# Optimization experiments

Measured on AMD Instinct MI355X. Metric: run time of the kernel, lower is better.

The kernel has to match this reference:

```python
import jax, jax.numpy as jnp
import numpy as np

NUM_USERS = 50000
NUM_ITEMS = 50000
EMBED_DIM = 128
NUM_LAYERS = 3
NUM_EDGES = 600000
N_NODES = NUM_USERS + NUM_ITEMS


def setup_inputs() -> dict:
    key = jax.random.key(0)
    k1, k2, k3, k4, k5 = jax.random.split(key, 5)
    edge_index = jax.random.randint(k1, (2, NUM_EDGES), 0, N_NODES, dtype=jnp.int64 if jax.config.x64_enabled else jnp.int32)
    user_emb = jax.random.normal(k2, (NUM_USERS, EMBED_DIM), jnp.float32) * 0.1
    item_emb = jax.random.normal(k3, (NUM_ITEMS, EMBED_DIM), jnp.float32) * 0.1
    Wa = jax.random.normal(k4, (NUM_LAYERS, 2 * EMBED_DIM, 1), jnp.float32) * 0.05
    ba = jnp.zeros((NUM_LAYERS, 1), jnp.float32)
    Wg = jax.random.normal(k5, (NUM_LAYERS, 2 * EMBED_DIM, EMBED_DIM), jnp.float32) * 0.05
    bg = jnp.zeros((NUM_LAYERS, EMBED_DIM), jnp.float32)
    return {"edge_index": edge_index, "user_emb": user_emb, "item_emb": item_emb,
            "Wa": Wa, "ba": ba, "Wg": Wg, "bg": bg}


def reference(edge_index, user_emb, item_emb, Wa, ba, Wg, bg):
    U = user_emb.shape[0]
    N = U + item_emb.shape[0]
    src, dst = edge_index[0], edge_index[1]
    x = jnp.concatenate([user_emb, item_emb], axis=0)  # [N, d]
    for l in range(Wa.shape[0]):
        src_emb = x[src]                                # [E, d] gather
        dst_emb = x[dst]                                # [E, d] gather
        cat = jnp.concatenate([src_emb, dst_emb], 1)    # [E, 2d]
        att = jax.nn.sigmoid(cat @ Wa[l] + ba[l])       # [E, 1]
        # attention-weighted scatter-sum over destination node (zeros for isolated nodes)
        agg = jax.ops.segment_sum(src_emb * att, dst, num_segments=N)  # [N, d]
        x = jax.nn.relu(jnp.concatenate([x, agg], 1) @ Wg[l] + bg[l])  # [N, d]
    return x[:U], x[U:]
```

## Files before the change

kernel.cpp:

```cpp
#include <hip/hip_runtime.h>
#include <cstddef>
#include <cstdint>

#define NUSERS 50000
#define NITEMS 50000
#define NNODES 100000
#define DIM    128
#define NLAYERS 3
#define NEDGES 600000
#define NPAD 100096

#define EBLK  8192
#define NBLK  74
#define NBUCK 782

#define PRO_CONCAT 6250
#define PRO_WG     48
#define PRO_TOTAL  (PRO_CONCAT + PRO_WG + NBLK)

typedef __attribute__((ext_vector_type(8))) short short8;
typedef __attribute__((ext_vector_type(4))) float f32x4;

__device__ __forceinline__ float bf_lo(unsigned u) { return __uint_as_float(u << 16); }
__device__ __forceinline__ float bf_hi(unsigned u) { return __uint_as_float(u & 0xffff0000u); }
__device__ __forceinline__ unsigned short f2bf(float f) {
    unsigned b = __float_as_uint(f);
    return (unsigned short)((b + 0x7fffu + ((b >> 16) & 1u)) >> 16);
}
__device__ __forceinline__ unsigned pack2(float lo, float hi) {
    return ((unsigned)f2bf(hi) << 16) | (unsigned)f2bf(lo);
}

__device__ __forceinline__ void async16(const void* g, void* l) {
    __builtin_amdgcn_global_load_lds(
        (const __attribute__((address_space(1))) unsigned int*)(uintptr_t)g,
        (__attribute__((address_space(3))) unsigned int*)(unsigned int)(uintptr_t)l,
        16, 0, 0);
}

__global__ __launch_bounds__(256) void prologue_kernel(
        const float* __restrict__ ue, const float* __restrict__ ie,
        const float* __restrict__ Wa, const float* __restrict__ ba,
        const float* __restrict__ Wg, const int* __restrict__ dst,
        unsigned short* __restrict__ xb,
        float* __restrict__ a_src, float* __restrict__ a_dst,
        unsigned short* __restrict__ Bf, unsigned* __restrict__ counts) {
    __shared__ unsigned hist[NBUCK];
    const int blk = blockIdx.x;

    if (blk < PRO_CONCAT) {
        const int n = blk * 16 + (threadIdx.x >> 4);
        if (n >= NNODES) return;
        const int sub = threadIdx.x & 15;
        const float* r = (n < NUSERS) ? (ue + (size_t)n * DIM)
                                      : (ie + (size_t)(n - NUSERS) * DIM);
        const float4 v0 = *(const float4*)(r + sub * 8);
        const float4 v1 = *(const float4*)(r + sub * 8 + 4);
        const float4 wl0 = *(const float4*)(Wa + sub * 8);
        const float4 wl1 = *(const float4*)(Wa + sub * 8 + 4);
        const float4 wh0 = *(const float4*)(Wa + DIM + sub * 8);
        const float4 wh1 = *(const float4*)(Wa + DIM + sub * 8 + 4);

        uint4 o;
        o.x = pack2(v0.x, v0.y);
        o.y = pack2(v0.z, v0.w);
        o.z = pack2(v1.x, v1.y);
        o.w = pack2(v1.z, v1.w);
        *(uint4*)(xb + (size_t)n * DIM + sub * 8) = o;

        float ps = v0.x * wl0.x + v0.y * wl0.y + v0.z * wl0.z + v0.w * wl0.w
                 + v1.x * wl1.x + v1.y * wl1.y + v1.z * wl1.z + v1.w * wl1.w;
        float pd = v0.x * wh0.x + v0.y * wh0.y + v0.z * wh0.z + v0.w * wh0.w
                 + v1.x * wh1.x + v1.y * wh1.y + v1.z * wh1.z + v1.w * wh1.w;
        #pragma unroll
        for (int off = 1; off < 16; off <<= 1) {
            ps += __shfl_xor(ps, off);
            pd += __shfl_xor(pd, off);
        }
        if (sub == 0) { a_src[n] = ps; a_dst[n] = pd + ba[0]; }
    } else if (blk < PRO_CONCAT + PRO_WG) {
        const int tid = (blk - PRO_CONCAT) * 256 + threadIdx.x;
        if (tid >= NLAYERS * 4096) return;
        const int l    = tid >> 12;
        const int slot = tid & 4095;
        const int lane = slot & 63;
        const int t2   = slot >> 6;
        const int nf   = t2 & 3;
        const int t3   = t2 >> 2;
        const int ks   = t3 & 7;
        const int nb   = t3 >> 3;
        const int col  = nb * 64 + nf * 16 + (lane & 15);
        const int k0   = ks * 32 + (lane >> 4) * 8;
        const float* wsrc = Wg + (size_t)l * 256 * DIM;
        unsigned short o[8];
        #pragma unroll
        for (int j = 0; j < 8; ++j) o[j] = f2bf(wsrc[(size_t)(k0 + j) * DIM + col]);
        *(short8*)(Bf + (size_t)tid * 8) = *(short8*)o;
    } else {
        const int bblk = blk - PRO_CONCAT - PRO_WG;
        for (int i = threadIdx.x; i < NBUCK; i += 256) hist[i] = 0;
        __syncthreads();
        const int base = bblk * EBLK;
        const int end  = (base + EBLK < NEDGES) ? base + EBLK : NEDGES;
        for (int e = base + threadIdx.x; e < end; e += 256)
            atomicAdd(&hist[dst[e] >> 7], 1u);
        __syncthreads();
        for (int i = threadIdx.x; i < NBUCK; i += 256)
            counts[(size_t)bblk * NBUCK + i] = hist[i];
    }
}

__global__ __launch_bounds__(256) void scan_blocks_kernel(
        unsigned* __restrict__ counts, unsigned* __restrict__ totals) {
    const int b = blockIdx.x * 4 + (threadIdx.x >> 6);
    if (b >= NBUCK) return;
    const int l = threadIdx.x & 63;

    const unsigned c0 = counts[(size_t)l * NBUCK + b];
    const unsigned c1 = (64 + l < NBLK)
                        ? counts[(size_t)(64 + l) * NBUCK + b] : 0;

    unsigned s0 = c0, s1 = c1;
    #pragma unroll
    for (int o = 1; o < 64; o <<= 1) {
        const unsigned t0 = (unsigned)__shfl_up((int)s0, o);
        const unsigned t1 = (unsigned)__shfl_up((int)s1, o);
        if (l >= o) { s0 += t0; s1 += t1; }
    }
    const unsigned tot0 = (unsigned)__shfl((int)s0, 63);
    const unsigned tot1 = (unsigned)__shfl((int)s1, NBLK - 65);

    counts[(size_t)l * NBUCK + b] = s0 - c0;
    if (64 + l < NBLK)
        counts[(size_t)(64 + l) * NBUCK + b] = tot0 + s1 - c1;
    if (l == 0) totals[b] = tot0 + tot1;
}

__global__ __launch_bounds__(1024) void bucketbase_kernel(
        const unsigned* __restrict__ totals, unsigned* __restrict__ bucketbase) {
    const int b = threadIdx.x;
    const unsigned v = (b < NBUCK) ? totals[b] : 0u;
    const int lane = b & 63, w = b >> 6;
    unsigned s = v;
    #pragma unroll
    for (int o = 1; o < 64; o <<= 1) {
        const unsigned t = (unsigned)__shfl_up((int)s, o);
        if (lane >= o) s += t;
    }
    __shared__ unsigned wsum[16];
    if (lane == 63) wsum[w] = s;
    __syncthreads();
    unsigned add = 0;
    #pragma unroll
    for (int j = 0; j < 15; ++j) if (w > j) add += wsum[j];
    if (b < NBUCK) bucketbase[b] = s + add - v;
    if (b == NBUCK - 1) bucketbase[NBUCK] = s + add;
}

__global__ __launch_bounds__(256) void bin_scatter_kernel(
        const int* __restrict__ src, const int* __restrict__ dst,
        const unsigned* __restrict__ counts, const unsigned* __restrict__ bucketbase,
        unsigned* __restrict__ pairs) {
    __shared__ unsigned off[NBUCK];
    for (int i = threadIdx.x; i < NBUCK; i += 256)
        off[i] = bucketbase[i] + counts[(size_t)blockIdx.x * NBUCK + i];
    __syncthreads();
    const int base = blockIdx.x * EBLK;
    const int end  = (base + EBLK < NEDGES) ? base + EBLK : NEDGES;
    for (int e = base + threadIdx.x; e < end; e += 256) {
        const int d = dst[e];
        const unsigned pos = atomicAdd(&off[d >> 7], 1u);
        pairs[pos] = ((unsigned)(d & 127) << 17) | (unsigned)src[e];
    }
}

__global__ __launch_bounds__(256) void bucket_csr_kernel(
        const unsigned* __restrict__ pairs, const unsigned* __restrict__ bucketbase,
        int* __restrict__ row_start, int* __restrict__ csr_src) {
    __shared__ unsigned deg[128], fill[128], wtot[2];
    const int b = blockIdx.x;
    const unsigned seg0 = bucketbase[b], seg1 = bucketbase[b + 1];
    const int t = threadIdx.x;
    if (t < 128) deg[t] = 0;
    __syncthreads();
    for (unsigned i = seg0 + t; i < seg1; i += 256)
        atomicAdd(&deg[pairs[i] >> 17], 1u);
    __syncthreads();
    unsigned incl = 0, v = 0;
    if (t < 128) {
        v = deg[t];
        unsigned s = v;
        #pragma unroll
        for (int o = 1; o < 64; o <<= 1) {
            const unsigned tmp = (unsigned)__shfl_up((int)s, o);
            if ((t & 63) >= o) s += tmp;
        }
        if ((t & 63) == 63) wtot[t >> 6] = s;
        incl = s;
    }
    __syncthreads();
    if (t < 128) {
        if (t >= 64) incl += wtot[0];
        const unsigned excl = incl - v;
        fill[t] = excl;
        const int node = b * 128 + t;
        if (node < NNODES) row_start[node] = (int)(seg0 + excl);
    }
    __syncthreads();
    for (unsigned i = seg0 + t; i < seg1; i += 256) {
        const unsigned p = pairs[i];
        const unsigned r = atomicAdd(&fill[p >> 17], 1u);
        csr_src[seg0 + r] = (int)(p & 0x1ffffu);
    }
    if (b == 0 && t == 0) row_start[NNODES] = NEDGES;
}

__global__ __launch_bounds__(256) void pull_agg_kernel(
        const int* __restrict__ row_start, const int* __restrict__ csr_src,
        const float* __restrict__ a_src, const float* __restrict__ a_dst,
        const unsigned short* __restrict__ xb, unsigned short* __restrict__ aggb) {
    const int n = blockIdx.x * 16 + (threadIdx.x >> 4);
    if (n >= NNODES) return;
    const int lane = threadIdx.x & 63;
    const int sub  = lane & 15;
    const int qb   = lane & 48;
    const int beg = row_start[n], end = row_start[n + 1];
    const float adst = a_dst[n];

    float a0 = 0, a1 = 0, a2 = 0, a3 = 0, a4 = 0, a5 = 0, a6 = 0, a7 = 0;

    for (int base = beg; base < end; base += 16) {
        const int rem = end - base;
        const int cnt = rem < 16 ? rem : 16;
        int   idx_l = 0;
        float att_l = 0.0f;
        if (sub < cnt) {
            idx_l = csr_src[base + sub];
            att_l = 1.0f / (1.0f + __expf(-(a_src[idx_l] + adst)));
        }
        int i = 0;
        for (; i + 3 < cnt; i += 4) {
            const int   s0 = __shfl(idx_l, qb + i);
            const int   s1 = __shfl(idx_l, qb + i + 1);
            const int   s2 = __shfl(idx_l, qb + i + 2);
            const int   s3 = __shfl(idx_l, qb + i + 3);
            const float w0 = __shfl(att_l, qb + i);
            const float w1 = __shfl(att_l, qb + i + 1);
            const float w2 = __shfl(att_l, qb + i + 2);
            const float w3 = __shfl(att_l, qb + i + 3);
            const uint4 u0 = *(const uint4*)(xb + (size_t)s0 * DIM + sub * 8);
            const uint4 u1 = *(const uint4*)(xb + (size_t)s1 * DIM + sub * 8);
            const uint4 u2 = *(const uint4*)(xb + (size_t)s2 * DIM + sub * 8);
            const uint4 u3 = *(const uint4*)(xb + (size_t)s3 * DIM + sub * 8);
            a0 += bf_lo(u0.x) * w0 + bf_lo(u1.x) * w1 + bf_lo(u2.x) * w2 + bf_lo(u3.x) * w3;
            a1 += bf_hi(u0.x) * w0 + bf_hi(u1.x) * w1 + bf_hi(u2.x) * w2 + bf_hi(u3.x) * w3;
            a2 += bf_lo(u0.y) * w0 + bf_lo(u1.y) * w1 + bf_lo(u2.y) * w2 + bf_lo(u3.y) * w3;
            a3 += bf_hi(u0.y) * w0 + bf_hi(u1.y) * w1 + bf_hi(u2.y) * w2 + bf_hi(u3.y) * w3;
            a4 += bf_lo(u0.z) * w0 + bf_lo(u1.z) * w1 + bf_lo(u2.z) * w2 + bf_lo(u3.z) * w3;
            a5 += bf_hi(u0.z) * w0 + bf_hi(u1.z) * w1 + bf_hi(u2.z) * w2 + bf_hi(u3.z) * w3;
            a6 += bf_lo(u0.w) * w0 + bf_lo(u1.w) * w1 + bf_lo(u2.w) * w2 + bf_lo(u3.w) * w3;
            a7 += bf_hi(u0.w) * w0 + bf_hi(u1.w) * w1 + bf_hi(u2.w) * w2 + bf_hi(u3.w) * w3;
        }
        for (; i < cnt; ++i) {
            const int   s = __shfl(idx_l, qb + i);
            const float w = __shfl(att_l, qb + i);
            const uint4 u = *(const uint4*)(xb + (size_t)s * DIM + sub * 8);
            a0 += bf_lo(u.x) * w;  a1 += bf_hi(u.x) * w;
            a2 += bf_lo(u.y) * w;  a3 += bf_hi(u.y) * w;
            a4 += bf_lo(u.z) * w;  a5 += bf_hi(u.z) * w;
            a6 += bf_lo(u.w) * w;  a7 += bf_hi(u.w) * w;
        }
    }

    uint4 o;
    o.x = pack2(a0, a1);
    o.y = pack2(a2, a3);
    o.z = pack2(a4, a5);
    o.w = pack2(a6, a7);
    *(uint4*)(aggb + (size_t)n * DIM + sub * 8) = o;
}

__global__ __launch_bounds__(256, 7) void gemm_mfma_kernel(
        unsigned short* __restrict__ xb, const unsigned short* __restrict__ aggb,
        const unsigned short* __restrict__ bfr, const float* __restrict__ bg,
        const float* __restrict__ wa_next, const float* __restrict__ ba_next,
        float* __restrict__ a_src, float* __restrict__ a_dst,
        float* __restrict__ xout_f32, int write_f32, int do_dots) {
    __shared__ unsigned short At[2][32 * 128];
    __shared__ float psS[4][32], psD[4][32];

    const int tid  = threadIdx.x;
    const int lane = tid & 63;
    const int wid  = tid >> 6;
    const int mbase = blockIdx.x * 32;

    #pragma unroll
    for (int h = 0; h < 2; ++h) {
        const unsigned short* s = h ? aggb : xb;
        #pragma unroll
        for (int i = 0; i < 2; ++i) {
            const int lrow = i * 16 + wid * 4 + (lane >> 4);
            const int c    = (lane & 15) ^ (lrow & 7);
            async16(s + (size_t)(mbase + lrow) * DIM + c * 8,
                    &At[h][(i * 16 + wid * 4) * 128]);
        }
    }

    const int l16 = lane & 15, kq = lane >> 4;
    const unsigned short* bfw = bfr + (size_t)(wid >> 1) * (8 * 4 * 64 * 8);
    const int nfo = (wid & 1) * 2;

    f32x4 acc[2][2] = {};

    asm volatile("s_waitcnt vmcnt(2)" ::: "memory");
    __builtin_amdgcn_s_barrier();

    #pragma unroll
    for (int ks = 0; ks < 8; ++ks) {
        if (ks == 4) {
            asm volatile("s_waitcnt vmcnt(0)" ::: "memory");
            __builtin_amdgcn_s_barrier();
        }
        const int h = ks >> 2, ksl = ks & 3;
        short8 b[2], a[2];
        #pragma unroll
        for (int nf = 0; nf < 2; ++nf)
            b[nf] = *(const short8*)(bfw + ((size_t)(ks * 4 + nfo + nf) * 64 + lane) * 8);
        #pragma unroll
        for (int mf = 0; mf < 2; ++mf) {
            const int row   = mf * 16 + l16;
            const int chunk = (ksl * 4 + kq) ^ (row & 7);
            a[mf] = *(const short8*)&At[h][row * 128 + chunk * 8];
        }
        #pragma unroll
        for (int mf = 0; mf < 2; ++mf)
            #pragma unroll
            for (int nf = 0; nf < 2; ++nf)
                acc[mf][nf] = __builtin_amdgcn_mfma_f32_16x16x32_bf16(
                    a[mf], b[nf], acc[mf][nf], 0, 0, 0);
    }

    const int rsub = kq * 4;
    float waS[2] = {0, 0}, waD[2] = {0, 0}, bias[2];
    #pragma unroll
    for (int nf = 0; nf < 2; ++nf) {
        const int col = wid * 32 + nf * 16 + l16;
        bias[nf] = bg[col];
        if (do_dots) { waS[nf] = wa_next[col]; waD[nf] = wa_next[DIM + col]; }
    }
    #pragma unroll
    for (int mf = 0; mf < 2; ++mf) {
        #pragma unroll
        for (int j = 0; j < 4; ++j) {
            const int row = mbase + mf * 16 + rsub + j;
            float s = 0.0f, d = 0.0f;
            #pragma unroll
            for (int nf = 0; nf < 2; ++nf) {
                const int col = wid * 32 + nf * 16 + l16;
                const float v = fmaxf(acc[mf][nf][j] + bias[nf], 0.0f);
                if (write_f32) {
                    xout_f32[(size_t)row * DIM + col] = v;
                } else {
                    const unsigned short bv = f2bf(v);
                    const unsigned pb = (unsigned)(unsigned short)__shfl_xor((int)bv, 1);
                    if (!(l16 & 1))
                        *(unsigned*)(xb + (size_t)row * DIM + col) =
                            (unsigned)bv | (pb << 16);
                }
                s += v * waS[nf];
                d += v * waD[nf];
            }
            if (do_dots) {
                #pragma unroll
                for (int off = 1; off < 16; off <<= 1) {
                    s += __shfl_xor(s, off);
                    d += __shfl_xor(d, off);
                }
                if (l16 == 0) {
                    const int rl = mf * 16 + rsub + j;
                    psS[wid][rl] = s;
                    psD[wid][rl] = d;
                }
            }
        }
    }
    if (do_dots) {
        __syncthreads();
        if (tid < 32) {
            const int row = mbase + tid;
            a_src[row] = psS[0][tid] + psS[1][tid] + psS[2][tid] + psS[3][tid];
            a_dst[row] = psD[0][tid] + psD[1][tid] + psD[2][tid] + psD[3][tid]
                       + ba_next[0];
        }
    }
}

extern "C" void kernel_launch(void* const* d_in, const int* in_sizes, int n_in,
                              void* d_out, int out_size, void* d_ws, size_t ws_size,
                              hipStream_t stream) {
    const int*   edge = (const int*)d_in[0];
    const float* ue   = (const float*)d_in[1];
    const float* ie   = (const float*)d_in[2];
    const float* Wa   = (const float*)d_in[3];
    const float* ba   = (const float*)d_in[4];
    const float* Wg   = (const float*)d_in[5];
    const float* bg   = (const float*)d_in[6];

    const int* src = edge;
    const int* dst = edge + NEDGES;

    float* x = (float*)d_out;

    unsigned short* xb   = (unsigned short*)d_ws;
    unsigned short* aggb = xb + (size_t)NPAD * DIM;
    unsigned short* bfr  = aggb + (size_t)NPAD * DIM;
    float* a_src      = (float*)(bfr + NLAYERS * 32768);
    float* a_dst      = a_src + NPAD;
    int*   row_start  = (int*)(a_dst + NPAD);
    int*   csr_src    = row_start + NPAD + 256;
    unsigned* pairs   = (unsigned*)(csr_src + NEDGES);
    unsigned* counts  = pairs + NEDGES;
    unsigned* totals  = counts + (size_t)NBLK * NBUCK;
    unsigned* bbase   = totals + NBUCK;

    prologue_kernel<<<PRO_TOTAL, 256, 0, stream>>>(
        ue, ie, Wa, ba, Wg, dst, xb, a_src, a_dst, bfr, counts);

    scan_blocks_kernel<<<(NBUCK + 3) / 4, 256, 0, stream>>>(counts, totals);
    bucketbase_kernel<<<1, 1024, 0, stream>>>(totals, bbase);
    bin_scatter_kernel<<<NBLK, 256, 0, stream>>>(src, dst, counts, bbase, pairs);
    bucket_csr_kernel<<<NBUCK, 256, 0, stream>>>(pairs, bbase, row_start, csr_src);

    const int gemm_blocks = NNODES / 32;
    const int pull_blocks = (NNODES + 15) / 16;
    for (int l = 0; l < NLAYERS; ++l) {
        pull_agg_kernel<<<pull_blocks, 256, 0, stream>>>(
            row_start, csr_src, a_src, a_dst, xb, aggb);
        const int last = (l == NLAYERS - 1);
        gemm_mfma_kernel<<<gemm_blocks, 256, 0, stream>>>(
            xb, aggb, bfr + (size_t)l * 32768, bg + (size_t)l * DIM,
            Wa + (size_t)(l + 1 < NLAYERS ? l + 1 : 0) * 256,
            ba + (l + 1 < NLAYERS ? l + 1 : 0),
            a_src, a_dst, x, last ? 1 : 0, last ? 0 : 1);
    }
}
```

Before: 214.7 us.

## Fuse attention pull aggregation into per-layer GEMM kernel with ping-pong buffers

Merges the pull-based attention aggregation and the MFMA GEMM into a single per-layer kernel. Each block aggregates its own 32 destination rows straight into shared memory instead of writing an agg buffer to global memory and reading it back. To avoid read/write hazards on x and the attention scalars, it ping-pongs between two bf16 x buffers and two sets of a_src/a_dst arrays. This removes three kernel launches and the agg round trip. In exchange the gather phase now runs inside a block shaped for the GEMM, with lower occupancy and a full barrier before the matrix multiply.

```diff
diff --git a/kernel.cpp b/kernel.cpp
--- a/kernel.cpp
+++ b/kernel.cpp
@@ -215,77 +215,15 @@
     if (b == 0 && t == 0) row_start[NNODES] = NEDGES;
 }
 
-__global__ __launch_bounds__(256) void pull_agg_kernel(
+__global__ __launch_bounds__(256, 6) void fused_layer_kernel(
+        const unsigned short* __restrict__ xin,
         const int* __restrict__ row_start, const int* __restrict__ csr_src,
         const float* __restrict__ a_src, const float* __restrict__ a_dst,
-        const unsigned short* __restrict__ xb, unsigned short* __restrict__ aggb) {
-    const int n = blockIdx.x * 16 + (threadIdx.x >> 4);
-    if (n >= NNODES) return;
-    const int lane = threadIdx.x & 63;
-    const int sub  = lane & 15;
-    const int qb   = lane & 48;
-    const int beg = row_start[n], end = row_start[n + 1];
-    const float adst = a_dst[n];
-
-    float a0 = 0, a1 = 0, a2 = 0, a3 = 0, a4 = 0, a5 = 0, a6 = 0, a7 = 0;
-
-    for (int base = beg; base < end; base += 16) {
-        const int rem = end - base;
-        const int cnt = rem < 16 ? rem : 16;
-        int   idx_l = 0;
-        float att_l = 0.0f;
-        if (sub < cnt) {
-            idx_l = csr_src[base + sub];
-            att_l = 1.0f / (1.0f + __expf(-(a_src[idx_l] + adst)));
-        }
-        int i = 0;
-        for (; i + 3 < cnt; i += 4) {
-            const int   s0 = __shfl(idx_l, qb + i);
-            const int   s1 = __shfl(idx_l, qb + i + 1);
-            const int   s2 = __shfl(idx_l, qb + i + 2);
-            const int   s3 = __shfl(idx_l, qb + i + 3);
-            const float w0 = __shfl(att_l, qb + i);
-            const float w1 = __shfl(att_l, qb + i + 1);
-            const float w2 = __shfl(att_l, qb + i + 2);
-            const float w3 = __shfl(att_l, qb + i + 3);
-            const uint4 u0 = *(const uint4*)(xb + (size_t)s0 * DIM + sub * 8);
-            const uint4 u1 = *(const uint4*)(xb + (size_t)s1 * DIM + sub * 8);
-            const uint4 u2 = *(const uint4*)(xb + (size_t)s2 * DIM + sub * 8);
-            const uint4 u3 = *(const uint4*)(xb + (size_t)s3 * DIM + sub * 8);
-            a0 += bf_lo(u0.x) * w0 + bf_lo(u1.x) * w1 + bf_lo(u2.x) * w2 + bf_lo(u3.x) * w3;
-            a1 += bf_hi(u0.x) * w0 + bf_hi(u1.x) * w1 + bf_hi(u2.x) * w2 + bf_hi(u3.x) * w3;
-            a2 += bf_lo(u0.y) * w0 + bf_lo(u1.y) * w1 + bf_lo(u2.y) * w2 + bf_lo(u3.y) * w3;
-            a3 += bf_hi(u0.y) * w0 + bf_hi(u1.y) * w1 + bf_hi(u2.y) * w2 + bf_hi(u3.y) * w3;
-            a4 += bf_lo(u0.z) * w0 + bf_lo(u1.z) * w1 + bf_lo(u2.z) * w2 + bf_lo(u3.z) * w3;
-            a5 += bf_hi(u0.z) * w0 + bf_hi(u1.z) * w1 + bf_hi(u2.z) * w2 + bf_hi(u3.z) * w3;
-            a6 += bf_lo(u0.w) * w0 + bf_lo(u1.w) * w1 + bf_lo(u2.w) * w2 + bf_lo(u3.w) * w3;
-            a7 += bf_hi(u0.w) * w0 + bf_hi(u1.w) * w1 + bf_hi(u2.w) * w2 + bf_hi(u3.w) * w3;
-        }
-        for (; i < cnt; ++i) {
-            const int   s = __shfl(idx_l, qb + i);
-            const float w = __shfl(att_l, qb + i);
-            const uint4 u = *(const uint4*)(xb + (size_t)s * DIM + sub * 8);
-            a0 += bf_lo(u.x) * w;  a1 += bf_hi(u.x) * w;
-            a2 += bf_lo(u.y) * w;  a3 += bf_hi(u.y) * w;
-            a4 += bf_lo(u.z) * w;  a5 += bf_hi(u.z) * w;
-            a6 += bf_lo(u.w) * w;  a7 += bf_hi(u.w) * w;
-        }
-    }
-
-    uint4 o;
-    o.x = pack2(a0, a1);
-    o.y = pack2(a2, a3);
-    o.z = pack2(a4, a5);
-    o.w = pack2(a6, a7);
-    *(uint4*)(aggb + (size_t)n * DIM + sub * 8) = o;
-}
-
-__global__ __launch_bounds__(256, 7) void gemm_mfma_kernel(
-        unsigned short* __restrict__ xb, const unsigned short* __restrict__ aggb,
         const unsigned short* __restrict__ bfr, const float* __restrict__ bg,
         const float* __restrict__ wa_next, const float* __restrict__ ba_next,
-        float* __restrict__ a_src, float* __restrict__ a_dst,
-        float* __restrict__ xout_f32, int write_f32, int do_dots) {
+        float* __restrict__ a_src_next, float* __restrict__ a_dst_next,
+        float* __restrict__ xout_f32, unsigned short* __restrict__ xout_bf,
+        int write_f32, int do_dots) {
     __shared__ unsigned short At[2][32 * 128];
     __shared__ float psS[4][32], psD[4][32];
 
@@ -295,16 +233,77 @@
     const int mbase = blockIdx.x * 32;
 
     #pragma unroll
-    for (int h = 0; h < 2; ++h) {
-        const unsigned short* s = h ? aggb : xb;
-        #pragma unroll
-        for (int i = 0; i < 2; ++i) {
-            const int lrow = i * 16 + wid * 4 + (lane >> 4);
-            const int c    = (lane & 15) ^ (lrow & 7);
-            async16(s + (size_t)(mbase + lrow) * DIM + c * 8,
-                    &At[h][(i * 16 + wid * 4) * 128]);
-        }
-    }
+    for (int i = 0; i < 2; ++i) {
+        const int lrow = i * 16 + wid * 4 + (lane >> 4);
+        const int c    = (lane & 15) ^ (lrow & 7);
+        async16(xin + (size_t)(mbase + lrow) * DIM + c * 8,
+                &At[0][(i * 16 + wid * 4) * 128]);
+    }
+
+    {
+        const int q   = tid >> 4;
+        const int sub = lane & 15;
+        const int qb  = lane & 48;
+        #pragma unroll
+        for (int it = 0; it < 2; ++it) {
+            const int n = mbase + it * 16 + q;
+            const int beg = row_start[n], end = row_start[n + 1];
+            const float adst = a_dst[n];
+            float a0 = 0, a1 = 0, a2 = 0, a3 = 0, a4 = 0, a5 = 0, a6 = 0, a7 = 0;
+            for (int base = beg; base < end; base += 16) {
+                const int rem = end - base;
+                const int cnt = rem < 16 ? rem : 16;
+                int   idx_l = 0;
+                float att_l = 0.0f;
+                if (sub < cnt) {
+                    idx_l = csr_src[base + sub];
+                    att_l = 1.0f / (1.0f + __expf(-(a_src[idx_l] + adst)));
+                }
+                int i = 0;
+                for (; i + 3 < cnt; i += 4) {
+                    const int   s0 = __shfl(idx_l, qb + i);
+                    const int   s1 = __shfl(idx_l, qb + i + 1);
+                    const int   s2 = __shfl(idx_l, qb + i + 2);
+                    const int   s3 = __shfl(idx_l, qb + i + 3);
+                    const float w0 = __shfl(att_l, qb + i);
+                    const float w1 = __shfl(att_l, qb + i + 1);
+                    const float w2 = __shfl(att_l, qb + i + 2);
+                    const float w3 = __shfl(att_l, qb + i + 3);
+                    const uint4 u0 = *(const uint4*)(xin + (size_t)s0 * DIM + sub * 8);
+                    const uint4 u1 = *(const uint4*)(xin + (size_t)s1 * DIM + sub * 8);
+                    const uint4 u2 = *(const uint4*)(xin + (size_t)s2 * DIM + sub * 8);
+                    const uint4 u3 = *(const uint4*)(xin + (size_t)s3 * DIM + sub * 8);
+                    a0 += bf_lo(u0.x) * w0 + bf_lo(u1.x) * w1 + bf_lo(u2.x) * w2 + bf_lo(u3.x) * w3;
+                    a1 += bf_hi(u0.x) * w0 + bf_hi(u1.x) * w1 + bf_hi(u2.x) * w2 + bf_hi(u3.x) * w3;
+                    a2 += bf_lo(u0.y) * w0 + bf_lo(u1.y) * w1 + bf_lo(u2.y) * w2 + bf_lo(u3.y) * w3;
+                    a3 += bf_hi(u0.y) * w0 + bf_hi(u1.y) * w1 + bf_hi(u2.y) * w2 + bf_hi(u3.y) * w3;
+                    a4 += bf_lo(u0.z) * w0 + bf_lo(u1.z) * w1 + bf_lo(u2.z) * w2 + bf_lo(u3.z) * w3;
+                    a5 += bf_hi(u0.z) * w0 + bf_hi(u1.z) * w1 + bf_hi(u2.z) * w2 + bf_hi(u3.z) * w3;
+                    a6 += bf_lo(u0.w) * w0 + bf_lo(u1.w) * w1 + bf_lo(u2.w) * w2 + bf_lo(u3.w) * w3;
+                    a7 += bf_hi(u0.w) * w0 + bf_hi(u1.w) * w1 + bf_hi(u2.w) * w2 + bf_hi(u3.w) * w3;
+                }
+                for (; i < cnt; ++i) {
+                    const int   s = __shfl(idx_l, qb + i);
+                    const float w = __shfl(att_l, qb + i);
+                    const uint4 u = *(const uint4*)(xin + (size_t)s * DIM + sub * 8);
+                    a0 += bf_lo(u.x) * w;  a1 += bf_hi(u.x) * w;
+                    a2 += bf_lo(u.y) * w;  a3 += bf_hi(u.y) * w;
+                    a4 += bf_lo(u.z) * w;  a5 += bf_hi(u.z) * w;
+                    a6 += bf_lo(u.w) * w;  a7 += bf_hi(u.w) * w;
+                }
+            }
+            uint4 o;
+            o.x = pack2(a0, a1);
+            o.y = pack2(a2, a3);
+            o.z = pack2(a4, a5);
+            o.w = pack2(a6, a7);
+            const int rl = it * 16 + q;
+            *(uint4*)&At[1][rl * 128 + ((sub ^ (rl & 7)) << 3)] = o;
+        }
+    }
+
+    asm volatile("s_waitcnt vmcnt(0) lgkmcnt(0)" ::: "memory");
+    __builtin_amdgcn_s_barrier();
 
     const int l16 = lane & 15, kq = lane >> 4;
     const unsigned short* bfw = bfr + (size_t)(wid >> 1) * (8 * 4 * 64 * 8);
@@ -312,15 +311,8 @@
 
     f32x4 acc[2][2] = {};
 
-    asm volatile("s_waitcnt vmcnt(2)" ::: "memory");
-    __builtin_amdgcn_s_barrier();
-
     #pragma unroll
     for (int ks = 0; ks < 8; ++ks) {
-        if (ks == 4) {
-            asm volatile("s_waitcnt vmcnt(0)" ::: "memory");
-            __builtin_amdgcn_s_barrier();
-        }
         const int h = ks >> 2, ksl = ks & 3;
         short8 b[2], a[2];
         #pragma unroll
@@ -364,7 +356,7 @@
                     const unsigned short bv = f2bf(v);
                     const unsigned pb = (unsigned)(unsigned short)__shfl_xor((int)bv, 1);
                     if (!(l16 & 1))
-                        *(unsigned*)(xb + (size_t)row * DIM + col) =
+                        *(unsigned*)(xout_bf + (size_t)row * DIM + col) =
                             (unsigned)bv | (pb << 16);
                 }
                 s += v * waS[nf];
@@ -388,9 +380,9 @@
         __syncthreads();
         if (tid < 32) {
             const int row = mbase + tid;
-            a_src[row] = psS[0][tid] + psS[1][tid] + psS[2][tid] + psS[3][tid];
-            a_dst[row] = psD[0][tid] + psD[1][tid] + psD[2][tid] + psD[3][tid]
-                       + ba_next[0];
+            a_src_next[row] = psS[0][tid] + psS[1][tid] + psS[2][tid] + psS[3][tid];
+            a_dst_next[row] = psD[0][tid] + psD[1][tid] + psD[2][tid] + psD[3][tid]
+                            + ba_next[0];
         }
     }
 }
@@ -411,12 +403,14 @@
 
     float* x = (float*)d_out;
 
-    unsigned short* xb   = (unsigned short*)d_ws;
-    unsigned short* aggb = xb + (size_t)NPAD * DIM;
-    unsigned short* bfr  = aggb + (size_t)NPAD * DIM;
-    float* a_src      = (float*)(bfr + NLAYERS * 32768);
-    float* a_dst      = a_src + NPAD;
-    int*   row_start  = (int*)(a_dst + NPAD);
+    unsigned short* xb0  = (unsigned short*)d_ws;
+    unsigned short* xb1  = xb0 + (size_t)NPAD * DIM;
+    unsigned short* bfr  = xb1 + (size_t)NPAD * DIM;
+    float* aSA        = (float*)(bfr + NLAYERS * 32768);
+    float* aDA        = aSA + NPAD;
+    float* aSB        = aDA + NPAD;
+    float* aDB        = aSB + NPAD;
+    int*   row_start  = (int*)(aDB + NPAD);
     int*   csr_src    = row_start + NPAD + 256;
     unsigned* pairs   = (unsigned*)(csr_src + NEDGES);
     unsigned* counts  = pairs + NEDGES;
@@ -424,23 +418,25 @@
     unsigned* bbase   = totals + NBUCK;
 
     prologue_kernel<<<PRO_TOTAL, 256, 0, stream>>>(
-        ue, ie, Wa, ba, Wg, dst, xb, a_src, a_dst, bfr, counts);
+        ue, ie, Wa, ba, Wg, dst, xb0, aSA, aDA, bfr, counts);
 
     scan_blocks_kernel<<<(NBUCK + 3) / 4, 256, 0, stream>>>(counts, totals);
     bucketbase_kernel<<<1, 1024, 0, stream>>>(totals, bbase);
     bin_scatter_kernel<<<NBLK, 256, 0, stream>>>(src, dst, counts, bbase, pairs);
     bucket_csr_kernel<<<NBUCK, 256, 0, stream>>>(pairs, bbase, row_start, csr_src);
 
-    const int gemm_blocks = NNODES / 32;
-    const int pull_blocks = (NNODES + 15) / 16;
-    for (int l = 0; l < NLAYERS; ++l) {
-        pull_agg_kernel<<<pull_blocks, 256, 0, stream>>>(
-            row_start, csr_src, a_src, a_dst, xb, aggb);
-        const int last = (l == NLAYERS - 1);
-        gemm_mfma_kernel<<<gemm_blocks, 256, 0, stream>>>(
-            xb, aggb, bfr + (size_t)l * 32768, bg + (size_t)l * DIM,
-            Wa + (size_t)(l + 1 < NLAYERS ? l + 1 : 0) * 256,
-            ba + (l + 1 < NLAYERS ? l + 1 : 0),
-            a_src, a_dst, x, last ? 1 : 0, last ? 0 : 1);
-    }
-}
+    const int blocks = NNODES / 32;
+
+    fused_layer_kernel<<<blocks, 256, 0, stream>>>(
+        xb0, row_start, csr_src, aSA, aDA,
+        bfr, bg, Wa + 256, ba + 1, aSB, aDB,
+        x, xb1, 0, 1);
+    fused_layer_kernel<<<blocks, 256, 0, stream>>>(
+        xb1, row_start, csr_src, aSB, aDB,
+        bfr + 32768, bg + DIM, Wa + 512, ba + 2, aSA, aDA,
+        x, xb0, 0, 1);
+    fused_layer_kernel<<<blocks, 256, 0, stream>>>(
+        xb0, row_start, csr_src, aSA, aDA,
+        bfr + 65536, bg + 2 * DIM, Wa, ba, aSB, aDB,
+        x, xb1, 1, 0);
+}
```

New measurement: 188.2 us (median of 2 runs). 12.4% less time.
